# Kernel optimization log

Measured on AMD Instinct MI355X. Metric: run time of the kernel, lower is better.

The kernel has to match this reference:

```python
import jax, jax.numpy as jnp
from jax import lax
import numpy as np

# --- config (torchvision Mask R-CNN RPN / RoIAlign defaults) ---
IMG = 800.0        # image size (square)
STRIDE = 4.0       # FPN level stride -> feature 200x200
K_PRE = 2000       # pre-NMS top-k proposals
K_POST = 512       # post-NMS proposals kept
IOU_THR = 0.7      # RPN NMS IoU threshold
OUT = 7            # RoIAlign output size
SR = 2             # RoIAlign sampling ratio
SCALE = 1.0 / STRIDE
BBOX_XFORM_CLIP = 4.135166556742356  # log(1000/16)


def setup_inputs() -> dict:
    key = jax.random.key(0)
    k1, k2, k3 = jax.random.split(key, 3)
    C, H, W = 256, 200, 200
    feature = jax.random.normal(k1, (C, H, W), jnp.float32)
    # anchor grid: 3 sizes per location, stride 4 (proper geometric anchors)
    sizes = np.array([32.0, 64.0, 128.0], np.float32)
    ys, xs = np.meshgrid(np.arange(H, dtype=np.float32) * STRIDE,
                         np.arange(W, dtype=np.float32) * STRIDE, indexing='ij')
    ctr = np.stack([xs, ys], axis=-1).reshape(-1, 1, 2)            # [HW,1,2] (x,y)
    half = np.stack([sizes / 2, sizes / 2], axis=-1)[None]          # [1,3,2]
    anchors = np.concatenate([ctr - half + 0 * half, ctr + half], axis=-1)
    anchors = np.broadcast_to(np.concatenate([ctr - half, ctr + half], -1),
                              (H * W, 3, 4)).reshape(-1, 4).astype(np.float32)
    N = anchors.shape[0]  # 120000
    objectness = jax.random.normal(k2, (N,), jnp.float32)
    deltas = jax.random.normal(k3, (N, 4), jnp.float32) * 0.1
    return {"feature": feature, "objectness": objectness,
            "deltas": deltas, "anchors": jnp.asarray(anchors)}


def decode_boxes(deltas, anchors):
    w = anchors[:, 2] - anchors[:, 0]
    h = anchors[:, 3] - anchors[:, 1]
    cx = anchors[:, 0] + 0.5 * w
    cy = anchors[:, 1] + 0.5 * h
    dx, dy = deltas[:, 0], deltas[:, 1]
    dw = jnp.minimum(deltas[:, 2], BBOX_XFORM_CLIP)
    dh = jnp.minimum(deltas[:, 3], BBOX_XFORM_CLIP)
    pcx = dx * w + cx
    pcy = dy * h + cy
    pw = jnp.exp(dw) * w
    ph = jnp.exp(dh) * h
    boxes = jnp.stack([pcx - 0.5 * pw, pcy - 0.5 * ph,
                       pcx + 0.5 * pw, pcy + 0.5 * ph], axis=-1)
    return jnp.clip(boxes, 0.0, IMG)


def pairwise_iou(b):  # b: [K,4]
    area = (b[:, 2] - b[:, 0]) * (b[:, 3] - b[:, 1])
    lt = jnp.maximum(b[:, None, :2], b[None, :, :2])
    rb = jnp.minimum(b[:, None, 2:], b[None, :, 2:])
    wh = jnp.maximum(rb - lt, 0.0)
    inter = wh[..., 0] * wh[..., 1]
    return inter / (area[:, None] + area[None, :] - inter + 1e-6)


def nms_suppress(boxes_sorted, iou_thr):
    # boxes sorted by descending score; returns keep mask [K]
    K = boxes_sorted.shape[0]
    iou = pairwise_iou(boxes_sorted)
    js = jnp.arange(K)
    def body(i, supp):
        row = (iou[i] > iou_thr) & (js > i)
        return jnp.where(supp[i], supp, supp | row)
    supp = lax.fori_loop(0, K, body, jnp.zeros((K,), bool))
    return ~supp


def roi_align(feature, boxes):
    # feature: [C,H,W]; boxes: [M,4] in image coords; aligned=False variant
    C, H, W = feature.shape
    P = OUT * SR
    def one(box):
        x1, y1, x2, y2 = box[0] * SCALE, box[1] * SCALE, box[2] * SCALE, box[3] * SCALE
        rw = jnp.maximum(x2 - x1, 1.0)
        rh = jnp.maximum(y2 - y1, 1.0)
        idx = jnp.arange(P, dtype=feature.dtype) + 0.5
        ys = y1 + idx * (rh / P)   # [P]
        xs = x1 + idx * (rw / P)
        yy, xx = jnp.meshgrid(ys, xs, indexing='ij')     # [P,P]
        y = jnp.clip(yy, 0.0, H - 1.0)
        x = jnp.clip(xx, 0.0, W - 1.0)
        y0 = jnp.floor(y).astype(jnp.int32)
        x0 = jnp.floor(x).astype(jnp.int32)
        y1i = jnp.minimum(y0 + 1, H - 1)
        x1i = jnp.minimum(x0 + 1, W - 1)
        ly = y - y0.astype(feature.dtype)
        lx = x - x0.astype(feature.dtype)
        v00 = feature[:, y0, x0]    # [C,P,P]
        v01 = feature[:, y0, x1i]
        v10 = feature[:, y1i, x0]
        v11 = feature[:, y1i, x1i]
        val = (v00 * (1 - ly) * (1 - lx) + v01 * (1 - ly) * lx
               + v10 * ly * (1 - lx) + v11 * ly * lx)  # [C,P,P]
        return val.reshape(C, OUT, SR, OUT, SR).mean(axis=(2, 4))  # [C,7,7]
    return jax.vmap(one)(boxes)


def reference(feature, objectness, deltas, anchors):
    boxes = decode_boxes(deltas, anchors)                    # [N,4]
    scores, idx = lax.top_k(objectness, K_PRE)               # pre-NMS top-k
    cand = boxes[idx]                                        # [K_PRE,4] sorted
    keep = nms_suppress(cand, IOU_THR)                       # [K_PRE] bool
    masked = jnp.where(keep, scores, -jnp.inf)
    _, fidx = lax.top_k(masked, K_POST)                      # post-NMS top-k
    final_boxes = cand[fidx]                                 # [K_POST,4]
    valid = keep[fidx].astype(feature.dtype)                 # [K_POST]
    roi = roi_align(feature, final_boxes)                    # [K_POST,256,7,7]
    return roi * valid[:, None, None, None]
```

## Files before the change

kernel.cpp:

```cpp
#include <hip/hip_runtime.h>
#include <cstdint>
#include <cstddef>

#define N_ANCH   120000
#define K_PRE    2000
#define K_POST   512
#define CAP      4096
#define NWORD    32
#define HBINS    4096
#define IOU_THR  0.7f
#define IMGF     800.0f
#define CLIPV    4.135166556742356f
#define FH       200
#define FW       200
#define FC       256
#define SCALE    0.25f

#define TROWS    96
#define NTILE    21
#define CH       8

#define CG       16
#define TPE      4

typedef unsigned long long u64;
typedef float f2u __attribute__((ext_vector_type(2), aligned(4)));

struct Ws {
    uint32_t T;
    uint32_t cnt;
    int32_t  nk;
    uint32_t pad;
    u64      combo[CAP];
    float4   cand[K_PRE];
    int      rows[K_POST];
    u64      mask[(size_t)K_PRE * NWORD];
};

__device__ inline uint32_t fkey(float f) {
    uint32_t u = __float_as_uint(f);
    return (u & 0x80000000u) ? ~u : (u | 0x80000000u);
}

__global__ __launch_bounds__(1024) void zero_k(Ws* __restrict__ ws) {
    uint32_t* h = (uint32_t*)ws->mask;
    for (int i = threadIdx.x; i < HBINS; i += 1024) h[i] = 0u;
    if (threadIdx.x == 0) { ws->cnt = 0u; ws->nk = 0; ws->T = 0u; }
}

__global__ __launch_bounds__(256) void hist_k(const float* __restrict__ obj,
                                              uint32_t* __restrict__ hist) {
    __shared__ uint32_t h[HBINS];
    for (int i = threadIdx.x; i < HBINS; i += 256) h[i] = 0u;
    __syncthreads();
    const float4* o4 = (const float4*)obj;
    for (int i = blockIdx.x * 256 + threadIdx.x; i < N_ANCH / 4; i += gridDim.x * 256) {
        float4 v = o4[i];
        atomicAdd(&h[fkey(v.x) >> 20], 1u);
        atomicAdd(&h[fkey(v.y) >> 20], 1u);
        atomicAdd(&h[fkey(v.z) >> 20], 1u);
        atomicAdd(&h[fkey(v.w) >> 20], 1u);
    }
    __syncthreads();
    for (int i = threadIdx.x; i < HBINS; i += 256)
        if (h[i]) atomicAdd(&hist[i], h[i]);
}

__global__ __launch_bounds__(256) void gather_k(const float* __restrict__ obj,
                                                const uint32_t* __restrict__ hist,
                                                Ws* __restrict__ ws) {
    __shared__ uint32_t wsum[4];
    __shared__ uint32_t sT;
    const int tid = threadIdx.x;
    const int lane = tid & 63, wave = tid >> 6;
    uint32_t c[16]; uint32_t s = 0;
#pragma unroll
    for (int k = 0; k < 16; ++k) { c[k] = hist[HBINS - 1 - (16 * tid + k)]; s += c[k]; }
    uint32_t incl = s;
    for (int off = 1; off < 64; off <<= 1) {
        uint32_t t = __shfl_up(incl, off);
        if (lane >= off) incl += t;
    }
    if (lane == 63) wsum[wave] = incl;
    __syncthreads();
    uint32_t wpre = 0;
    for (int w2 = 0; w2 < wave; ++w2) wpre += wsum[w2];
    uint32_t before = wpre + incl - s;
#pragma unroll
    for (int k = 0; k < 16; ++k) {
        uint32_t after = before + c[k];
        if (before < K_PRE && after >= K_PRE)
            sT = (uint32_t)(HBINS - 1 - (16 * tid + k)) << 20;
        before = after;
    }
    __syncthreads();
    const uint32_t T = sT;
    int i = blockIdx.x * 256 + tid;
    if (i >= N_ANCH / 4) return;
    float4 v = ((const float4*)obj)[i];
    float vals[4] = {v.x, v.y, v.z, v.w};
#pragma unroll
    for (int k = 0; k < 4; ++k) {
        uint32_t u = fkey(vals[k]);
        if (u >= T) {
            uint32_t pos = atomicAdd(&ws->cnt, 1u);
            if (pos < CAP)
                ws->combo[pos] = ((u64)(~u) << 32) | (uint32_t)(4 * i + k);
        }
    }
}

__global__ __launch_bounds__(256) void rank_decode_k(const float* __restrict__ deltas,
                                                     const float* __restrict__ anchors,
                                                     Ws* __restrict__ ws) {
    __shared__ u64 sc[CAP];
    const int tid = threadIdx.x;
    int M = (int)ws->cnt;
    if (M > CAP) M = CAP;
    const int ebase = blockIdx.x * (256 / TPE);
    if (ebase >= M) return;
    for (int e = tid; e < M; e += 256) sc[e] = ws->combo[e];
    __syncthreads();
    const int gid = ebase + tid / TPE;
    const int sub = tid & (TPE - 1);
    if (gid >= M) return;
    const u64 mine = sc[gid];
    int cnt = 0;
    int j = sub;
    for (; j + 3 * TPE < M; j += 4 * TPE) {
        u64 a = sc[j], b = sc[j + TPE], c = sc[j + 2 * TPE], d = sc[j + 3 * TPE];
        cnt += (int)(a < mine) + (int)(b < mine) + (int)(c < mine) + (int)(d < mine);
    }
    for (; j < M; j += TPE) cnt += (int)(sc[j] < mine);
    cnt += __shfl_xor(cnt, 1);
    cnt += __shfl_xor(cnt, 2);
    if (sub == 0 && cnt < K_PRE) {
        const uint32_t idx = (uint32_t)(mine & 0xFFFFFFFFull);
        float a0 = anchors[idx * 4 + 0], a1 = anchors[idx * 4 + 1];
        float a2 = anchors[idx * 4 + 2], a3 = anchors[idx * 4 + 3];
        float d0 = deltas[idx * 4 + 0],  d1 = deltas[idx * 4 + 1];
        float d2 = fminf(deltas[idx * 4 + 2], CLIPV);
        float d3 = fminf(deltas[idx * 4 + 3], CLIPV);
        float w = a2 - a0, h = a3 - a1;
        float cx = a0 + 0.5f * w, cy = a1 + 0.5f * h;
        float pcx = d0 * w + cx, pcy = d1 * h + cy;
        float pw = expf(d2) * w, ph = expf(d3) * h;
        float x1 = fminf(fmaxf(pcx - 0.5f * pw, 0.0f), IMGF);
        float y1 = fminf(fmaxf(pcy - 0.5f * ph, 0.0f), IMGF);
        float x2 = fminf(fmaxf(pcx + 0.5f * pw, 0.0f), IMGF);
        float y2 = fminf(fmaxf(pcy + 0.5f * ph, 0.0f), IMGF);
        ws->cand[cnt] = make_float4(x1, y1, x2, y2);
    }
}

__global__ __launch_bounds__(256) void nms_mask_k(Ws* __restrict__ ws) {
    const int i = blockIdx.x;
    const int lane = threadIdx.x & 63;
    const int wave = threadIdx.x >> 6;
    const float4 bi = ws->cand[i];
    const float ai = (bi.z - bi.x) * (bi.w - bi.y);
    for (int wd = wave; wd < NWORD; wd += 4) {
        int j = wd * 64 + lane;
        bool bit = false;
        if (j < K_PRE && j > i) {
            float4 bj = ws->cand[j];
            float aj = (bj.z - bj.x) * (bj.w - bj.y);
            float xx1 = fmaxf(bi.x, bj.x);
            float yy1 = fmaxf(bi.y, bj.y);
            float xx2 = fminf(bi.z, bj.z);
            float yy2 = fminf(bi.w, bj.w);
            float ww = fmaxf(xx2 - xx1, 0.0f);
            float hh = fmaxf(yy2 - yy1, 0.0f);
            float inter = ww * hh;
            float iou = inter / (ai + aj - inter + 1e-6f);
            bit = iou > IOU_THR;
        }
        u64 bal = __ballot(bit);
        if (lane == 0) ws->mask[(size_t)i * NWORD + wd] = bal;
    }
}

__global__ __launch_bounds__(512) void nms_scan_k(Ws* __restrict__ ws) {
    __shared__ __align__(16) u64 sbuf[2][TROWS * NWORD];
    __shared__ int s_stop;
    const int tid = threadIdx.x;
    const int lane = tid & 63;
    const int wave = tid >> 6;
    const int lmod = lane & 31;
    const u64* __restrict__ mask = ws->mask;

    {
        const ulonglong2* src = (const ulonglong2*)mask;
        ulonglong2* dst = (ulonglong2*)sbuf[0];
        for (int e = tid; e < TROWS * NWORD / 2; e += 512) dst[e] = src[e];
    }
    if (tid == 0) s_stop = 0;
    __syncthreads();

    u64 supp = 0ull;
    int kcnt = 0;
    int decided = 0;
    for (int t = 0; t < NTILE; ++t) {
        const int base = t * TROWS;
        const int nb = min(TROWS, K_PRE - base);
        if (wave == 0) {
            const u64* sm = sbuf[t & 1];
            u64 A[CH], B[CH];
#pragma unroll
            for (int b = 0; b < CH; ++b) A[b] = sm[b * NWORD + lmod];
            for (int s = 0; s < nb; s += 2 * CH) {
                const bool hasB = (s + CH) < nb;
                if (hasB) {
#pragma unroll
                    for (int b = 0; b < CH; ++b) B[b] = sm[(s + CH + b) * NWORD + lmod];
                }
                {
                    const int w = (base + s) >> 6;
                    const int bofs = (base + s) & 63;
                    u64 keptw = 0ull;
                    if (lane == w) {
                        u64 cur = supp;
#pragma unroll
                        for (int b = 0; b < CH; ++b) {
                            u64 bit = (cur >> (bofs + b)) & 1ull;
                            u64 sel = bit - 1ull;
                            cur |= A[b] & sel;
                            keptw |= sel & (1ull << b);
                        }
                        supp = cur;
                    }
                    u64 kb = __shfl(keptw, w);
                    kcnt += __popcll(kb);
#pragma unroll
                    for (int b = 0; b < CH; ++b) {
                        u64 sel = 0ull - ((kb >> b) & 1ull);
                        supp |= A[b] & sel;
                    }
                }
                if (hasB) {
                    if (s + 2 * CH < nb) {
#pragma unroll
                        for (int b = 0; b < CH; ++b)
                            A[b] = sm[(s + 2 * CH + b) * NWORD + lmod];
                    }
                    const int w = (base + s + CH) >> 6;
                    const int bofs = (base + s + CH) & 63;
                    u64 keptw = 0ull;
                    if (lane == w) {
                        u64 cur = supp;
#pragma unroll
                        for (int b = 0; b < CH; ++b) {
                            u64 bit = (cur >> (bofs + b)) & 1ull;
                            u64 sel = bit - 1ull;
                            cur |= B[b] & sel;
                            keptw |= sel & (1ull << b);
                        }
                        supp = cur;
                    }
                    u64 kb = __shfl(keptw, w);
                    kcnt += __popcll(kb);
#pragma unroll
                    for (int b = 0; b < CH; ++b) {
                        u64 sel = 0ull - ((kb >> b) & 1ull);
                        supp |= B[b] & sel;
                    }
                }
            }
            decided = base + nb;
            if (lane == 0 && kcnt >= K_POST) s_stop = 1;
        } else if (t + 1 < NTILE) {
            const int nbase = (t + 1) * TROWS;
            const int npairs = (min(TROWS, K_PRE - nbase) * NWORD) / 2;
            const ulonglong2* src = (const ulonglong2*)(mask + (size_t)nbase * NWORD);
            ulonglong2* dst = (ulonglong2*)sbuf[(t + 1) & 1];
            for (int e = tid - 64; e < npairs; e += 448) dst[e] = src[e];
        }
        __syncthreads();
        if (s_stop) break;
    }

    if (wave == 0) {
        u64 valid;
        if (lane < NWORD - 1)       valid = ~0ull;
        else if (lane == NWORD - 1) valid = (1ull << (K_PRE - (NWORD - 1) * 64)) - 1ull;
        else                        valid = 0ull;
        const int dw = decided - lane * 64;
        const u64 dmask = (dw <= 0) ? 0ull : ((dw >= 64) ? ~0ull : ((1ull << dw) - 1ull));
        u64 keepw = (~supp) & valid & dmask;
        int cnt = __popcll(keepw);
        int incl = cnt;
        for (int off = 1; off < 64; off <<= 1) {
            int t = __shfl_up(incl, off);
            if (lane >= off) incl += t;
        }
        int pos = incl - cnt;
        u64 kw = keepw;
        while (kw) {
            int b = __ffsll((unsigned long long)kw) - 1;
            kw &= kw - 1ull;
            if (pos < K_POST) ws->rows[pos] = lane * 64 + b;
            ++pos;
        }
        int total = __shfl(incl, 63);
        if (lane == 0) ws->nk = total;
        int start = total < K_POST ? total : K_POST;
        for (int r = start + lane; r < K_POST; r += 64) ws->rows[r] = -1;
    }
}

__global__ __launch_bounds__(256) void roi_k(const float* __restrict__ feat,
                                             const Ws* __restrict__ ws,
                                             float* __restrict__ out) {
    const int b = blockIdx.x;
    const int xcd = b & 7;
    const int s = b >> 3;
    const int r = s & (K_POST - 1);
    const int cg = xcd + 8 * (s >> 9);
    const int cbase = cg * CG;
    float* oblk = out + (size_t)r * (FC * 49) + (size_t)cbase * 49;
    const int row = ws->rows[r];
    const int tid = threadIdx.x;

    if (row < 0) {
        for (int e = tid; e < CG * 49; e += 256) oblk[e] = 0.0f;
        return;
    }
    if (tid >= 245) return;

    const int p = tid % 49;
    const int cslot = tid / 49;
    const int oy = p / 7, ox = p % 7;

    const float4 bx = ws->cand[row];
    const float x1 = bx.x * SCALE, y1 = bx.y * SCALE;
    const float x2 = bx.z * SCALE, y2 = bx.w * SCALE;
    const float rw = fmaxf(x2 - x1, 1.0f);
    const float rh = fmaxf(y2 - y1, 1.0f);
    const float stepx = rw / 14.0f;
    const float stepy = rh / 14.0f;

    int    off0[4], off1[4];
    float4 w4[4];
#pragma unroll
    for (int sub = 0; sub < 4; ++sub) {
        const int sy = sub >> 1, sx = sub & 1;
        float yy = y1 + ((float)(2 * oy + sy) + 0.5f) * stepy;
        float y = fminf(fmaxf(yy, 0.0f), (float)(FH - 1));
        float fy0 = floorf(y);
        int iy0 = (int)fy0;
        int iy1 = min(iy0 + 1, FH - 1);
        float ly = y - fy0;
        float xx = x1 + ((float)(2 * ox + sx) + 0.5f) * stepx;
        float x = fminf(fmaxf(xx, 0.0f), (float)(FW - 1));
        float fx0 = floorf(x);
        int ix0 = (int)fx0;
        float lx = x - fx0;
        float wxl, wxr; int base;
        if (ix0 >= FW - 1) { base = FW - 2; wxl = 0.0f; wxr = 1.0f; }
        else               { base = ix0;    wxl = 1.0f - lx; wxr = lx; }
        float wy0 = 1.0f - ly, wy1 = ly;
        off0[sub] = iy0 * FW + base;
        off1[sub] = iy1 * FW + base;
        w4[sub] = make_float4(wy0 * wxl * 0.25f, wy0 * wxr * 0.25f,
                              wy1 * wxl * 0.25f, wy1 * wxr * 0.25f);
    }

    const float* fb = feat + (size_t)cbase * (FH * FW);
    const float* f0 = fb + (size_t)cslot * (FH * FW);
    const float* f1 = fb + (size_t)(cslot + 5) * (FH * FW);
    const float* f2 = fb + (size_t)(cslot + 10) * (FH * FW);
    f2u r0[8], r1[8], r2[8], r3[8];
#pragma unroll
    for (int sub = 0; sub < 4; ++sub) {
        r0[2 * sub]     = *(const f2u*)(f0 + off0[sub]);
        r0[2 * sub + 1] = *(const f2u*)(f0 + off1[sub]);
    }
#pragma unroll
    for (int sub = 0; sub < 4; ++sub) {
        r1[2 * sub]     = *(const f2u*)(f1 + off0[sub]);
        r1[2 * sub + 1] = *(const f2u*)(f1 + off1[sub]);
    }
#pragma unroll
    for (int sub = 0; sub < 4; ++sub) {
        r2[2 * sub]     = *(const f2u*)(f2 + off0[sub]);
        r2[2 * sub + 1] = *(const f2u*)(f2 + off1[sub]);
    }
    const bool has4 = (cslot == 0);
    if (has4) {
        const float* f3 = fb + (size_t)15 * (FH * FW);
#pragma unroll
        for (int sub = 0; sub < 4; ++sub) {
            r3[2 * sub]     = *(const f2u*)(f3 + off0[sub]);
            r3[2 * sub + 1] = *(const f2u*)(f3 + off1[sub]);
        }
    }

    float a0 = 0.0f, a1 = 0.0f, a2 = 0.0f;
#pragma unroll
    for (int sub = 0; sub < 4; ++sub) {
        a0 += w4[sub].x * r0[2 * sub].x + w4[sub].y * r0[2 * sub].y
            + w4[sub].z * r0[2 * sub + 1].x + w4[sub].w * r0[2 * sub + 1].y;
    }
#pragma unroll
    for (int sub = 0; sub < 4; ++sub) {
        a1 += w4[sub].x * r1[2 * sub].x + w4[sub].y * r1[2 * sub].y
            + w4[sub].z * r1[2 * sub + 1].x + w4[sub].w * r1[2 * sub + 1].y;
    }
#pragma unroll
    for (int sub = 0; sub < 4; ++sub) {
        a2 += w4[sub].x * r2[2 * sub].x + w4[sub].y * r2[2 * sub].y
            + w4[sub].z * r2[2 * sub + 1].x + w4[sub].w * r2[2 * sub + 1].y;
    }
    oblk[cslot * 49 + p] = a0;
    oblk[(cslot + 5) * 49 + p] = a1;
    oblk[(cslot + 10) * 49 + p] = a2;

    if (has4) {
        float a3 = 0.0f;
#pragma unroll
        for (int sub = 0; sub < 4; ++sub) {
            a3 += w4[sub].x * r3[2 * sub].x + w4[sub].y * r3[2 * sub].y
                + w4[sub].z * r3[2 * sub + 1].x + w4[sub].w * r3[2 * sub + 1].y;
        }
        oblk[15 * 49 + p] = a3;
    }
}

extern "C" void kernel_launch(void* const* d_in, const int* in_sizes, int n_in,
                              void* d_out, int out_size, void* d_ws, size_t ws_size,
                              hipStream_t stream) {
    const float* feature    = (const float*)d_in[0];
    const float* objectness = (const float*)d_in[1];
    const float* deltas     = (const float*)d_in[2];
    const float* anchors    = (const float*)d_in[3];
    Ws* ws = (Ws*)d_ws;
    uint32_t* hist = (uint32_t*)ws->mask;
    float* out = (float*)d_out;

    hipLaunchKernelGGL(zero_k, dim3(1), dim3(1024), 0, stream, ws);
    hipLaunchKernelGGL(hist_k, dim3(256), dim3(256), 0, stream, objectness, hist);
    hipLaunchKernelGGL(gather_k, dim3((N_ANCH / 4 + 255) / 256), dim3(256), 0, stream,
                       objectness, hist, ws);
    hipLaunchKernelGGL(rank_decode_k, dim3(CAP / (256 / TPE)), dim3(256), 0, stream,
                       deltas, anchors, ws);
    hipLaunchKernelGGL(nms_mask_k, dim3(K_PRE), dim3(256), 0, stream, ws);
    hipLaunchKernelGGL(nms_scan_k, dim3(1), dim3(512), 0, stream, ws);
    hipLaunchKernelGGL(roi_k, dim3(16 * K_POST), dim3(256), 0, stream, feature, ws, out);
}
```

Measured before the change: 195.2 us.

## Fuse selection stages into one grid-synced kernel and merge mask with scan

Replaces the zero, histogram, gather and rank/decode kernels with a single 128-block kernel that uses global atomic-counter barriers between phases. The NMS mask and scan kernels are merged using a last-block-done pattern, where the final finishing block runs the sequential scan. This removes several kernel launches and the gaps between them. In exchange it relies on all 128 blocks being co-resident for the spin barriers, adds a memset, and reuses ws->T as the completion counter.

```diff
diff --git a/kernel.cpp b/kernel.cpp
--- a/kernel.cpp
+++ b/kernel.cpp
@@ -22,6 +22,7 @@
 
 #define CG       16
 #define TPE      4
+#define SEL_NB   128
 
 typedef unsigned long long u64;
 typedef float f2u __attribute__((ext_vector_type(2), aligned(4)));
@@ -42,153 +43,191 @@
     return (u & 0x80000000u) ? ~u : (u | 0x80000000u);
 }
 
-__global__ __launch_bounds__(1024) void zero_k(Ws* __restrict__ ws) {
-    uint32_t* h = (uint32_t*)ws->mask;
-    for (int i = threadIdx.x; i < HBINS; i += 1024) h[i] = 0u;
-    if (threadIdx.x == 0) { ws->cnt = 0u; ws->nk = 0; ws->T = 0u; }
-}
-
-__global__ __launch_bounds__(256) void hist_k(const float* __restrict__ obj,
-                                              uint32_t* __restrict__ hist) {
-    __shared__ uint32_t h[HBINS];
-    for (int i = threadIdx.x; i < HBINS; i += 256) h[i] = 0u;
-    __syncthreads();
-    const float4* o4 = (const float4*)obj;
-    for (int i = blockIdx.x * 256 + threadIdx.x; i < N_ANCH / 4; i += gridDim.x * 256) {
-        float4 v = o4[i];
-        atomicAdd(&h[fkey(v.x) >> 20], 1u);
-        atomicAdd(&h[fkey(v.y) >> 20], 1u);
-        atomicAdd(&h[fkey(v.z) >> 20], 1u);
-        atomicAdd(&h[fkey(v.w) >> 20], 1u);
-    }
-    __syncthreads();
-    for (int i = threadIdx.x; i < HBINS; i += 256)
-        if (h[i]) atomicAdd(&hist[i], h[i]);
-}
-
-__global__ __launch_bounds__(256) void gather_k(const float* __restrict__ obj,
-                                                const uint32_t* __restrict__ hist,
-                                                Ws* __restrict__ ws) {
-    __shared__ uint32_t wsum[4];
-    __shared__ uint32_t sT;
-    const int tid = threadIdx.x;
-    const int lane = tid & 63, wave = tid >> 6;
-    uint32_t c[16]; uint32_t s = 0;
-#pragma unroll
-    for (int k = 0; k < 16; ++k) { c[k] = hist[HBINS - 1 - (16 * tid + k)]; s += c[k]; }
-    uint32_t incl = s;
-    for (int off = 1; off < 64; off <<= 1) {
-        uint32_t t = __shfl_up(incl, off);
-        if (lane >= off) incl += t;
-    }
-    if (lane == 63) wsum[wave] = incl;
-    __syncthreads();
-    uint32_t wpre = 0;
-    for (int w2 = 0; w2 < wave; ++w2) wpre += wsum[w2];
-    uint32_t before = wpre + incl - s;
-#pragma unroll
-    for (int k = 0; k < 16; ++k) {
-        uint32_t after = before + c[k];
-        if (before < K_PRE && after >= K_PRE)
-            sT = (uint32_t)(HBINS - 1 - (16 * tid + k)) << 20;
-        before = after;
-    }
-    __syncthreads();
-    const uint32_t T = sT;
-    int i = blockIdx.x * 256 + tid;
-    if (i >= N_ANCH / 4) return;
-    float4 v = ((const float4*)obj)[i];
-    float vals[4] = {v.x, v.y, v.z, v.w};
-#pragma unroll
-    for (int k = 0; k < 4; ++k) {
-        uint32_t u = fkey(vals[k]);
-        if (u >= T) {
-            uint32_t pos = atomicAdd(&ws->cnt, 1u);
-            if (pos < CAP)
-                ws->combo[pos] = ((u64)(~u) << 32) | (uint32_t)(4 * i + k);
-        }
-    }
-}
-
-__global__ __launch_bounds__(256) void rank_decode_k(const float* __restrict__ deltas,
-                                                     const float* __restrict__ anchors,
-                                                     Ws* __restrict__ ws) {
-    __shared__ u64 sc[CAP];
-    const int tid = threadIdx.x;
-    int M = (int)ws->cnt;
-    if (M > CAP) M = CAP;
-    const int ebase = blockIdx.x * (256 / TPE);
-    if (ebase >= M) return;
-    for (int e = tid; e < M; e += 256) sc[e] = ws->combo[e];
-    __syncthreads();
-    const int gid = ebase + tid / TPE;
-    const int sub = tid & (TPE - 1);
-    if (gid >= M) return;
-    const u64 mine = sc[gid];
-    int cnt = 0;
-    int j = sub;
-    for (; j + 3 * TPE < M; j += 4 * TPE) {
-        u64 a = sc[j], b = sc[j + TPE], c = sc[j + 2 * TPE], d = sc[j + 3 * TPE];
-        cnt += (int)(a < mine) + (int)(b < mine) + (int)(c < mine) + (int)(d < mine);
-    }
-    for (; j < M; j += TPE) cnt += (int)(sc[j] < mine);
-    cnt += __shfl_xor(cnt, 1);
-    cnt += __shfl_xor(cnt, 2);
-    if (sub == 0 && cnt < K_PRE) {
-        const uint32_t idx = (uint32_t)(mine & 0xFFFFFFFFull);
-        float a0 = anchors[idx * 4 + 0], a1 = anchors[idx * 4 + 1];
-        float a2 = anchors[idx * 4 + 2], a3 = anchors[idx * 4 + 3];
-        float d0 = deltas[idx * 4 + 0],  d1 = deltas[idx * 4 + 1];
-        float d2 = fminf(deltas[idx * 4 + 2], CLIPV);
-        float d3 = fminf(deltas[idx * 4 + 3], CLIPV);
-        float w = a2 - a0, h = a3 - a1;
-        float cx = a0 + 0.5f * w, cy = a1 + 0.5f * h;
-        float pcx = d0 * w + cx, pcy = d1 * h + cy;
-        float pw = expf(d2) * w, ph = expf(d3) * h;
-        float x1 = fminf(fmaxf(pcx - 0.5f * pw, 0.0f), IMGF);
-        float y1 = fminf(fmaxf(pcy - 0.5f * ph, 0.0f), IMGF);
-        float x2 = fminf(fmaxf(pcx + 0.5f * pw, 0.0f), IMGF);
-        float y2 = fminf(fmaxf(pcy + 0.5f * ph, 0.0f), IMGF);
-        ws->cand[cnt] = make_float4(x1, y1, x2, y2);
-    }
-}
-
-__global__ __launch_bounds__(256) void nms_mask_k(Ws* __restrict__ ws) {
-    const int i = blockIdx.x;
-    const int lane = threadIdx.x & 63;
-    const int wave = threadIdx.x >> 6;
-    const float4 bi = ws->cand[i];
-    const float ai = (bi.z - bi.x) * (bi.w - bi.y);
-    for (int wd = wave; wd < NWORD; wd += 4) {
-        int j = wd * 64 + lane;
-        bool bit = false;
-        if (j < K_PRE && j > i) {
-            float4 bj = ws->cand[j];
-            float aj = (bj.z - bj.x) * (bj.w - bj.y);
-            float xx1 = fmaxf(bi.x, bj.x);
-            float yy1 = fmaxf(bi.y, bj.y);
-            float xx2 = fminf(bi.z, bj.z);
-            float yy2 = fminf(bi.w, bj.w);
-            float ww = fmaxf(xx2 - xx1, 0.0f);
-            float hh = fmaxf(yy2 - yy1, 0.0f);
-            float inter = ww * hh;
-            float iou = inter / (ai + aj - inter + 1e-6f);
-            bit = iou > IOU_THR;
-        }
-        u64 bal = __ballot(bit);
-        if (lane == 0) ws->mask[(size_t)i * NWORD + wd] = bal;
-    }
-}
-
-__global__ __launch_bounds__(512) void nms_scan_k(Ws* __restrict__ ws) {
+__device__ inline void dbar(uint32_t* ctr, uint32_t nb) {
+    __syncthreads();
+    if (threadIdx.x == 0) {
+        __threadfence();
+        atomicAdd(ctr, 1u);
+        while (__hip_atomic_load(ctr, __ATOMIC_RELAXED, __HIP_MEMORY_SCOPE_AGENT) < nb)
+            __builtin_amdgcn_s_sleep(2);
+        __threadfence();
+    }
+    __syncthreads();
+}
+
+union __align__(16) SelSmem {
+    uint32_t hist[HBINS];
+    struct { uint32_t wsum[4]; uint32_t sT; } res;
+    u64 sc[CAP];
+};
+
+__global__ __launch_bounds__(256) void sel_k(const float* __restrict__ obj,
+                                             const float* __restrict__ deltas,
+                                             const float* __restrict__ anchors,
+                                             Ws* __restrict__ ws) {
+    __shared__ SelSmem sm;
+    const int tid  = threadIdx.x;
+    const int bid  = blockIdx.x;
+    const int lane = tid & 63;
+    const int wave = tid >> 6;
+    uint32_t* hist = (uint32_t*)ws->mask;
+    uint32_t* bctr = hist + HBINS;
+
+    if (tid < HBINS / SEL_NB) hist[bid * (HBINS / SEL_NB) + tid] = 0u;
+    if (bid == 0 && tid == 0) { ws->cnt = 0u; ws->T = 0u; }
+
+    for (int i = tid; i < HBINS; i += 256) sm.hist[i] = 0u;
+    __syncthreads();
+    {
+        const float4* o4 = (const float4*)obj;
+        const int i = bid * 256 + tid;
+        if (i < N_ANCH / 4) {
+            float4 v = o4[i];
+            atomicAdd(&sm.hist[fkey(v.x) >> 20], 1u);
+            atomicAdd(&sm.hist[fkey(v.y) >> 20], 1u);
+            atomicAdd(&sm.hist[fkey(v.z) >> 20], 1u);
+            atomicAdd(&sm.hist[fkey(v.w) >> 20], 1u);
+        }
+    }
+    __syncthreads();
+
+    dbar(&bctr[0], SEL_NB);
+
+    for (int i = tid; i < HBINS; i += 256)
+        if (sm.hist[i]) atomicAdd(&hist[i], sm.hist[i]);
+
+    dbar(&bctr[1], SEL_NB);
+
+    {
+        uint32_t c[16]; uint32_t s = 0;
+#pragma unroll
+        for (int k = 0; k < 16; ++k) { c[k] = hist[HBINS - 1 - (16 * tid + k)]; s += c[k]; }
+        uint32_t incl = s;
+        for (int off = 1; off < 64; off <<= 1) {
+            uint32_t t = __shfl_up(incl, off);
+            if (lane >= off) incl += t;
+        }
+        __syncthreads();
+        if (lane == 63) sm.res.wsum[wave] = incl;
+        __syncthreads();
+        uint32_t wpre = 0;
+        for (int w2 = 0; w2 < wave; ++w2) wpre += sm.res.wsum[w2];
+        uint32_t before = wpre + incl - s;
+#pragma unroll
+        for (int k = 0; k < 16; ++k) {
+            uint32_t after = before + c[k];
+            if (before < K_PRE && after >= K_PRE)
+                sm.res.sT = (uint32_t)(HBINS - 1 - (16 * tid + k)) << 20;
+            before = after;
+        }
+        __syncthreads();
+        const uint32_t T = sm.res.sT;
+        const int i = bid * 256 + tid;
+        if (i < N_ANCH / 4) {
+            float4 v = ((const float4*)obj)[i];
+            float vals[4] = {v.x, v.y, v.z, v.w};
+#pragma unroll
+            for (int k = 0; k < 4; ++k) {
+                uint32_t u = fkey(vals[k]);
+                if (u >= T) {
+                    uint32_t pos = atomicAdd(&ws->cnt, 1u);
+                    if (pos < CAP)
+                        ws->combo[pos] = ((u64)(~u) << 32) | (uint32_t)(4 * i + k);
+                }
+            }
+        }
+    }
+
+    dbar(&bctr[2], SEL_NB);
+
+    {
+        int M = (int)ws->cnt;
+        if (M > CAP) M = CAP;
+        const int ebase = bid * (256 / TPE);
+        if (ebase >= M) return;
+        __syncthreads();
+        for (int e = tid; e < M; e += 256) sm.sc[e] = ws->combo[e];
+        __syncthreads();
+        const int gid = ebase + tid / TPE;
+        const int sub = tid & (TPE - 1);
+        if (gid >= M) return;
+        const u64 mine = sm.sc[gid];
+        int cnt = 0;
+        int j = sub;
+        for (; j + 3 * TPE < M; j += 4 * TPE) {
+            u64 a = sm.sc[j], b = sm.sc[j + TPE];
+            u64 c2 = sm.sc[j + 2 * TPE], d = sm.sc[j + 3 * TPE];
+            cnt += (int)(a < mine) + (int)(b < mine) + (int)(c2 < mine) + (int)(d < mine);
+        }
+        for (; j < M; j += TPE) cnt += (int)(sm.sc[j] < mine);
+        cnt += __shfl_xor(cnt, 1);
+        cnt += __shfl_xor(cnt, 2);
+        if (sub == 0 && cnt < K_PRE) {
+            const uint32_t idx = (uint32_t)(mine & 0xFFFFFFFFull);
+            float a0 = anchors[idx * 4 + 0], a1 = anchors[idx * 4 + 1];
+            float a2 = anchors[idx * 4 + 2], a3 = anchors[idx * 4 + 3];
+            float d0 = deltas[idx * 4 + 0],  d1 = deltas[idx * 4 + 1];
+            float d2 = fminf(deltas[idx * 4 + 2], CLIPV);
+            float d3 = fminf(deltas[idx * 4 + 3], CLIPV);
+            float w = a2 - a0, h = a3 - a1;
+            float cx = a0 + 0.5f * w, cy = a1 + 0.5f * h;
+            float pcx = d0 * w + cx, pcy = d1 * h + cy;
+            float pw = expf(d2) * w, ph = expf(d3) * h;
+            float x1 = fminf(fmaxf(pcx - 0.5f * pw, 0.0f), IMGF);
+            float y1 = fminf(fmaxf(pcy - 0.5f * ph, 0.0f), IMGF);
+            float x2 = fminf(fmaxf(pcx + 0.5f * pw, 0.0f), IMGF);
+            float y2 = fminf(fmaxf(pcy + 0.5f * ph, 0.0f), IMGF);
+            ws->cand[cnt] = make_float4(x1, y1, x2, y2);
+        }
+    }
+}
+
+__global__ __launch_bounds__(512) void mask_scan_k(Ws* __restrict__ ws) {
     __shared__ __align__(16) u64 sbuf[2][TROWS * NWORD];
     __shared__ int s_stop;
+    __shared__ int s_last;
     const int tid = threadIdx.x;
     const int lane = tid & 63;
     const int wave = tid >> 6;
+
+    {
+        const int i = blockIdx.x;
+        const float4 bi = ws->cand[i];
+        const float ai = (bi.z - bi.x) * (bi.w - bi.y);
+        for (int wd = wave; wd < NWORD; wd += 8) {
+            int j = wd * 64 + lane;
+            bool bit = false;
+            if (j < K_PRE && j > i) {
+                float4 bj = ws->cand[j];
+                float aj = (bj.z - bj.x) * (bj.w - bj.y);
+                float xx1 = fmaxf(bi.x, bj.x);
+                float yy1 = fmaxf(bi.y, bj.y);
+                float xx2 = fminf(bi.z, bj.z);
+                float yy2 = fminf(bi.w, bj.w);
+                float ww = fmaxf(xx2 - xx1, 0.0f);
+                float hh = fmaxf(yy2 - yy1, 0.0f);
+                float inter = ww * hh;
+                float iou = inter / (ai + aj - inter + 1e-6f);
+                bit = iou > IOU_THR;
+            }
+            u64 bal = __ballot(bit);
+            if (lane == 0) ws->mask[(size_t)i * NWORD + wd] = bal;
+        }
+    }
+
+    __syncthreads();
+    if (tid == 0) {
+        __threadfence();
+        uint32_t old = atomicAdd(&ws->T, 1u);
+        s_last = (old == K_PRE - 1) ? 1 : 0;
+    }
+    __syncthreads();
+    if (!s_last) return;
+    if (tid == 0) __threadfence();
+    __syncthreads();
+
     const int lmod = lane & 31;
     const u64* __restrict__ mask = ws->mask;
-
     {
         const ulonglong2* src = (const ulonglong2*)mask;
         ulonglong2* dst = (ulonglong2*)sbuf[0];
@@ -434,16 +473,12 @@
     const float* deltas     = (const float*)d_in[2];
     const float* anchors    = (const float*)d_in[3];
     Ws* ws = (Ws*)d_ws;
-    uint32_t* hist = (uint32_t*)ws->mask;
     float* out = (float*)d_out;
 
-    hipLaunchKernelGGL(zero_k, dim3(1), dim3(1024), 0, stream, ws);
-    hipLaunchKernelGGL(hist_k, dim3(256), dim3(256), 0, stream, objectness, hist);
-    hipLaunchKernelGGL(gather_k, dim3((N_ANCH / 4 + 255) / 256), dim3(256), 0, stream,
-                       objectness, hist, ws);
-    hipLaunchKernelGGL(rank_decode_k, dim3(CAP / (256 / TPE)), dim3(256), 0, stream,
-                       deltas, anchors, ws);
-    hipLaunchKernelGGL(nms_mask_k, dim3(K_PRE), dim3(256), 0, stream, ws);
-    hipLaunchKernelGGL(nms_scan_k, dim3(1), dim3(512), 0, stream, ws);
+    hipMemsetAsync((char*)d_ws + offsetof(Ws, mask) + (size_t)HBINS * 4, 0, 12, stream);
+
+    hipLaunchKernelGGL(sel_k, dim3(SEL_NB), dim3(256), 0, stream,
+                       objectness, deltas, anchors, ws);
+    hipLaunchKernelGGL(mask_scan_k, dim3(K_PRE), dim3(512), 0, stream, ws);
     hipLaunchKernelGGL(roi_k, dim3(16 * K_POST), dim3(256), 0, stream, feature, ws, out);
 }
```

Result: slower. 252.1 us (+29.2%).

## Fuse NMS scan with RoIAlign via progressive row publishing and spin-wait

Applied to the files above, without the earlier changes.

Merges the serial NMS scan kernel and the RoIAlign kernel into one launch. Block 0 runs the scan and, after each tile, publishes the kept rows found so far together with an atomic release counter. The remaining blocks spin on that counter until their row is ready, then run RoIAlign, so feature gathering overlaps the scan. RoI blocks now cover two channel groups with 512 threads each. This relies on block 0 being scheduled, or on enough other blocks finishing, to avoid deadlock, and the spinning blocks occupy compute units while they wait.

```diff
diff --git a/kernel.cpp b/kernel.cpp
--- a/kernel.cpp
+++ b/kernel.cpp
@@ -180,155 +180,182 @@
     }
 }
 
-__global__ __launch_bounds__(512) void nms_scan_k(Ws* __restrict__ ws) {
+__global__ __launch_bounds__(512) void scan_roi_k(const float* __restrict__ feat,
+                                                  Ws* __restrict__ ws,
+                                                  float* __restrict__ out) {
     __shared__ __align__(16) u64 sbuf[2][TROWS * NWORD];
     __shared__ int s_stop;
+    __shared__ int sRow;
     const int tid = threadIdx.x;
     const int lane = tid & 63;
     const int wave = tid >> 6;
-    const int lmod = lane & 31;
-    const u64* __restrict__ mask = ws->mask;
-
-    {
-        const ulonglong2* src = (const ulonglong2*)mask;
-        ulonglong2* dst = (ulonglong2*)sbuf[0];
-        for (int e = tid; e < TROWS * NWORD / 2; e += 512) dst[e] = src[e];
-    }
-    if (tid == 0) s_stop = 0;
-    __syncthreads();
-
-    u64 supp = 0ull;
-    int kcnt = 0;
-    int decided = 0;
-    for (int t = 0; t < NTILE; ++t) {
-        const int base = t * TROWS;
-        const int nb = min(TROWS, K_PRE - base);
-        if (wave == 0) {
-            const u64* sm = sbuf[t & 1];
-            u64 A[CH], B[CH];
-#pragma unroll
-            for (int b = 0; b < CH; ++b) A[b] = sm[b * NWORD + lmod];
-            for (int s = 0; s < nb; s += 2 * CH) {
-                const bool hasB = (s + CH) < nb;
-                if (hasB) {
-#pragma unroll
-                    for (int b = 0; b < CH; ++b) B[b] = sm[(s + CH + b) * NWORD + lmod];
+
+    if (blockIdx.x == 0) {
+        const int lmod = lane & 31;
+        const u64* __restrict__ mask = ws->mask;
+        {
+            const ulonglong2* src = (const ulonglong2*)mask;
+            ulonglong2* dst = (ulonglong2*)sbuf[0];
+            for (int e = tid; e < TROWS * NWORD / 2; e += 512) dst[e] = src[e];
+        }
+        if (tid == 0) s_stop = 0;
+        __syncthreads();
+
+        u64 supp = 0ull;
+        int pubtot = 0;
+        const u64 valid = (lane < NWORD - 1) ? ~0ull
+                        : (lane == NWORD - 1 ? ((1ull << (K_PRE - (NWORD - 1) * 64)) - 1ull)
+                                             : 0ull);
+        for (int t = 0; t < NTILE; ++t) {
+            const int base = t * TROWS;
+            const int nb = min(TROWS, K_PRE - base);
+            if (wave == 0) {
+                const u64* sm = sbuf[t & 1];
+                u64 A[CH], B[CH];
+#pragma unroll
+                for (int b = 0; b < CH; ++b) A[b] = sm[b * NWORD + lmod];
+                for (int s = 0; s < nb; s += 2 * CH) {
+                    const bool hasB = (s + CH) < nb;
+                    if (hasB) {
+#pragma unroll
+                        for (int b = 0; b < CH; ++b) B[b] = sm[(s + CH + b) * NWORD + lmod];
+                    }
+                    {
+                        const int w = (base + s) >> 6;
+                        const int bofs = (base + s) & 63;
+                        u64 keptw = 0ull;
+                        if (lane == w) {
+                            u64 cur = supp;
+#pragma unroll
+                            for (int b = 0; b < CH; ++b) {
+                                u64 bit = (cur >> (bofs + b)) & 1ull;
+                                u64 sel = bit - 1ull;
+                                cur |= A[b] & sel;
+                                keptw |= sel & (1ull << b);
+                            }
+                            supp = cur;
+                        }
+                        u64 kb = __shfl(keptw, w);
+#pragma unroll
+                        for (int b = 0; b < CH; ++b) {
+                            u64 sel = 0ull - ((kb >> b) & 1ull);
+                            supp |= A[b] & sel;
+                        }
+                    }
+                    if (hasB) {
+                        if (s + 2 * CH < nb) {
+#pragma unroll
+                            for (int b = 0; b < CH; ++b)
+                                A[b] = sm[(s + 2 * CH + b) * NWORD + lmod];
+                        }
+                        const int w = (base + s + CH) >> 6;
+                        const int bofs = (base + s + CH) & 63;
+                        u64 keptw = 0ull;
+                        if (lane == w) {
+                            u64 cur = supp;
+#pragma unroll
+                            for (int b = 0; b < CH; ++b) {
+                                u64 bit = (cur >> (bofs + b)) & 1ull;
+                                u64 sel = bit - 1ull;
+                                cur |= B[b] & sel;
+                                keptw |= sel & (1ull << b);
+                            }
+                            supp = cur;
+                        }
+                        u64 kb = __shfl(keptw, w);
+#pragma unroll
+                        for (int b = 0; b < CH; ++b) {
+                            u64 sel = 0ull - ((kb >> b) & 1ull);
+                            supp |= B[b] & sel;
+                        }
+                    }
                 }
                 {
-                    const int w = (base + s) >> 6;
-                    const int bofs = (base + s) & 63;
-                    u64 keptw = 0ull;
-                    if (lane == w) {
-                        u64 cur = supp;
-#pragma unroll
-                        for (int b = 0; b < CH; ++b) {
-                            u64 bit = (cur >> (bofs + b)) & 1ull;
-                            u64 sel = bit - 1ull;
-                            cur |= A[b] & sel;
-                            keptw |= sel & (1ull << b);
-                        }
-                        supp = cur;
-                    }
-                    u64 kb = __shfl(keptw, w);
-                    kcnt += __popcll(kb);
-#pragma unroll
-                    for (int b = 0; b < CH; ++b) {
-                        u64 sel = 0ull - ((kb >> b) & 1ull);
-                        supp |= A[b] & sel;
+                    const int w0 = lane << 6;
+                    int lo = base - w0;      if (lo < 0)  lo = 0;
+                    int hi = base + nb - w0; if (hi > 64) hi = 64;
+                    u64 rmask = 0ull;
+                    if (hi > lo) {
+                        u64 mh = (hi >= 64) ? ~0ull : ((1ull << hi) - 1ull);
+                        u64 ml = (lo <= 0) ? 0ull : ((1ull << lo) - 1ull);
+                        rmask = mh & ~ml;
+                    }
+                    u64 keepn = (~supp) & valid & rmask;
+                    int c = __popcll(keepn);
+                    int incl = c;
+                    for (int off = 1; off < 64; off <<= 1) {
+                        int tt = __shfl_up(incl, off);
+                        if (lane >= off) incl += tt;
+                    }
+                    int pos = pubtot + incl - c;
+                    u64 kw = keepn;
+                    while (kw) {
+                        int b = __ffsll((unsigned long long)kw) - 1;
+                        kw &= kw - 1ull;
+                        if (pos < K_POST)
+                            __hip_atomic_store(&ws->rows[pos], w0 + b,
+                                               __ATOMIC_RELAXED, __HIP_MEMORY_SCOPE_AGENT);
+                        ++pos;
+                    }
+                    pubtot += __shfl(incl, 63);
+                    int pr = pubtot < K_POST ? pubtot : K_POST;
+                    if (lane == 0) {
+                        __hip_atomic_store(&ws->T, (uint32_t)pr,
+                                           __ATOMIC_RELEASE, __HIP_MEMORY_SCOPE_AGENT);
+                        if (pubtot >= K_POST) s_stop = 1;
                     }
                 }
-                if (hasB) {
-                    if (s + 2 * CH < nb) {
-#pragma unroll
-                        for (int b = 0; b < CH; ++b)
-                            A[b] = sm[(s + 2 * CH + b) * NWORD + lmod];
-                    }
-                    const int w = (base + s + CH) >> 6;
-                    const int bofs = (base + s + CH) & 63;
-                    u64 keptw = 0ull;
-                    if (lane == w) {
-                        u64 cur = supp;
-#pragma unroll
-                        for (int b = 0; b < CH; ++b) {
-                            u64 bit = (cur >> (bofs + b)) & 1ull;
-                            u64 sel = bit - 1ull;
-                            cur |= B[b] & sel;
-                            keptw |= sel & (1ull << b);
-                        }
-                        supp = cur;
-                    }
-                    u64 kb = __shfl(keptw, w);
-                    kcnt += __popcll(kb);
-#pragma unroll
-                    for (int b = 0; b < CH; ++b) {
-                        u64 sel = 0ull - ((kb >> b) & 1ull);
-                        supp |= B[b] & sel;
-                    }
-                }
+            } else if (t + 1 < NTILE) {
+                const int nbase = (t + 1) * TROWS;
+                const int npairs = (min(TROWS, K_PRE - nbase) * NWORD) / 2;
+                const ulonglong2* src = (const ulonglong2*)(mask + (size_t)nbase * NWORD);
+                ulonglong2* dst = (ulonglong2*)sbuf[(t + 1) & 1];
+                for (int e = tid - 64; e < npairs; e += 448) dst[e] = src[e];
             }
-            decided = base + nb;
-            if (lane == 0 && kcnt >= K_POST) s_stop = 1;
-        } else if (t + 1 < NTILE) {
-            const int nbase = (t + 1) * TROWS;
-            const int npairs = (min(TROWS, K_PRE - nbase) * NWORD) / 2;
-            const ulonglong2* src = (const ulonglong2*)(mask + (size_t)nbase * NWORD);
-            ulonglong2* dst = (ulonglong2*)sbuf[(t + 1) & 1];
-            for (int e = tid - 64; e < npairs; e += 448) dst[e] = src[e];
-        }
-        __syncthreads();
-        if (s_stop) break;
-    }
-
-    if (wave == 0) {
-        u64 valid;
-        if (lane < NWORD - 1)       valid = ~0ull;
-        else if (lane == NWORD - 1) valid = (1ull << (K_PRE - (NWORD - 1) * 64)) - 1ull;
-        else                        valid = 0ull;
-        const int dw = decided - lane * 64;
-        const u64 dmask = (dw <= 0) ? 0ull : ((dw >= 64) ? ~0ull : ((1ull << dw) - 1ull));
-        u64 keepw = (~supp) & valid & dmask;
-        int cnt = __popcll(keepw);
-        int incl = cnt;
-        for (int off = 1; off < 64; off <<= 1) {
-            int t = __shfl_up(incl, off);
-            if (lane >= off) incl += t;
-        }
-        int pos = incl - cnt;
-        u64 kw = keepw;
-        while (kw) {
-            int b = __ffsll((unsigned long long)kw) - 1;
-            kw &= kw - 1ull;
-            if (pos < K_POST) ws->rows[pos] = lane * 64 + b;
-            ++pos;
-        }
-        int total = __shfl(incl, 63);
-        if (lane == 0) ws->nk = total;
-        int start = total < K_POST ? total : K_POST;
-        for (int r = start + lane; r < K_POST; r += 64) ws->rows[r] = -1;
-    }
-}
-
-__global__ __launch_bounds__(256) void roi_k(const float* __restrict__ feat,
-                                             const Ws* __restrict__ ws,
-                                             float* __restrict__ out) {
-    const int b = blockIdx.x;
-    const int xcd = b & 7;
-    const int s = b >> 3;
-    const int r = s & (K_POST - 1);
-    const int cg = xcd + 8 * (s >> 9);
+            __syncthreads();
+            if (s_stop) break;
+        }
+
+        if (wave == 0) {
+            for (int rr = pubtot + lane; rr < K_POST; rr += 64)
+                __hip_atomic_store(&ws->rows[rr], -1,
+                                   __ATOMIC_RELAXED, __HIP_MEMORY_SCOPE_AGENT);
+            if (lane == 0) {
+                ws->nk = pubtot;
+                __hip_atomic_store(&ws->T, (uint32_t)K_POST,
+                                   __ATOMIC_RELEASE, __HIP_MEMORY_SCOPE_AGENT);
+            }
+        }
+        return;
+    }
+
+    const int u = (int)blockIdx.x - 1;
+    const int r = u >> 3;
+    const int xcd = u & 7;
+    const int h = tid >> 8;
+    const int tid2 = tid & 255;
+    const int cg = xcd + 8 * h;
     const int cbase = cg * CG;
+
+    if (tid == 0) {
+        while (__hip_atomic_load(&ws->T, __ATOMIC_RELAXED, __HIP_MEMORY_SCOPE_AGENT)
+               <= (uint32_t)r)
+            __builtin_amdgcn_s_sleep(16);
+        (void)__hip_atomic_load(&ws->T, __ATOMIC_ACQUIRE, __HIP_MEMORY_SCOPE_AGENT);
+        sRow = __hip_atomic_load(&ws->rows[r], __ATOMIC_RELAXED, __HIP_MEMORY_SCOPE_AGENT);
+    }
+    __syncthreads();
+    const int row = sRow;
     float* oblk = out + (size_t)r * (FC * 49) + (size_t)cbase * 49;
-    const int row = ws->rows[r];
-    const int tid = threadIdx.x;
 
     if (row < 0) {
-        for (int e = tid; e < CG * 49; e += 256) oblk[e] = 0.0f;
+        for (int e = tid2; e < CG * 49; e += 256) oblk[e] = 0.0f;
         return;
     }
-    if (tid >= 245) return;
-
-    const int p = tid % 49;
-    const int cslot = tid / 49;
+    if (tid2 >= 245) return;
+
+    const int p = tid2 % 49;
+    const int cslot = tid2 / 49;
     const int oy = p / 7, ox = p % 7;
 
     const float4 bx = ws->cand[row];
@@ -444,6 +471,6 @@
     hipLaunchKernelGGL(rank_decode_k, dim3(CAP / (256 / TPE)), dim3(256), 0, stream,
                        deltas, anchors, ws);
     hipLaunchKernelGGL(nms_mask_k, dim3(K_PRE), dim3(256), 0, stream, ws);
-    hipLaunchKernelGGL(nms_scan_k, dim3(1), dim3(512), 0, stream, ws);
-    hipLaunchKernelGGL(roi_k, dim3(16 * K_POST), dim3(256), 0, stream, feature, ws, out);
-}
+    hipLaunchKernelGGL(scan_roi_k, dim3(1 + 8 * K_POST), dim3(512), 0, stream,
+                       feature, ws, out);
+}
```

New measurement: 200.8 us. 2.8% more time.

## Transpose feature map to HWC fused with histogram, use channel-vectorized RoIAlign

Applied to the files above, without the earlier changes.

Adds a kernel that transposes the CHW feature map into an HWC copy in workspace and also does the objectness histogram in the same launch. A new RoIAlign kernel reads float4 channel groups from the HWC layout for each bilinear corner, then stages the results in shared memory so the output writes are coalesced. The goal is to replace scattered per-channel gathers with contiguous vector loads. The cost is an extra full feature-map read and write (about 41 MB) on every call, and the path only runs when the workspace is large enough.

```diff
diff --git a/kernel.cpp b/kernel.cpp
--- a/kernel.cpp
+++ b/kernel.cpp
@@ -23,6 +23,7 @@
 #define CG       16
 #define TPE      4
 
+
 typedef unsigned long long u64;
 typedef float f2u __attribute__((ext_vector_type(2), aligned(4)));
 
@@ -46,6 +47,41 @@
     uint32_t* h = (uint32_t*)ws->mask;
     for (int i = threadIdx.x; i < HBINS; i += 1024) h[i] = 0u;
     if (threadIdx.x == 0) { ws->cnt = 0u; ws->nk = 0; ws->T = 0u; }
+}
+
+__global__ __launch_bounds__(256) void th_k(const float* __restrict__ feat,
+                                            const float* __restrict__ obj,
+                                            float* __restrict__ featT,
+                                            uint32_t* __restrict__ hist) {
+    __shared__ float tile[32][257];
+    __shared__ uint32_t h[HBINS];
+    const int tid = threadIdx.x, bid = blockIdx.x;
+
+    if (bid < 118) {
+        for (int i = tid; i < HBINS; i += 256) h[i] = 0u;
+        __syncthreads();
+        const int i = bid * 256 + tid;
+        if (i < N_ANCH / 4) {
+            float4 v = ((const float4*)obj)[i];
+            atomicAdd(&h[fkey(v.x) >> 20], 1u);
+            atomicAdd(&h[fkey(v.y) >> 20], 1u);
+            atomicAdd(&h[fkey(v.z) >> 20], 1u);
+            atomicAdd(&h[fkey(v.w) >> 20], 1u);
+        }
+        __syncthreads();
+        for (int i2 = tid; i2 < HBINS; i2 += 256)
+            if (h[i2]) atomicAdd(&hist[i2], h[i2]);
+    }
+
+    const int P0 = bid * 32;
+    const int pl = tid & 31, c0 = tid >> 5;
+#pragma unroll
+    for (int k = 0; k < 32; ++k)
+        tile[pl][k * 8 + c0] = feat[(size_t)(k * 8 + c0) * (FH * FW) + P0 + pl];
+    __syncthreads();
+#pragma unroll
+    for (int m = 0; m < 32; ++m)
+        featT[(size_t)(P0 + m) * FC + tid] = tile[m][tid];
 }
 
 __global__ __launch_bounds__(256) void hist_k(const float* __restrict__ obj,
@@ -308,6 +344,92 @@
     }
 }
 
+__global__ __launch_bounds__(256) void roi2_k(const float* __restrict__ featT,
+                                              const Ws* __restrict__ ws,
+                                              float* __restrict__ out) {
+    __shared__ float sout[CG * 49];
+    const int b = blockIdx.x;
+    const int xcd = b & 7;
+    const int s = b >> 3;
+    const int r = s & (K_POST - 1);
+    const int cg = xcd + 8 * (s >> 9);
+    const int cbase = cg * CG;
+    float* oblk = out + (size_t)r * (FC * 49) + (size_t)cbase * 49;
+    const int row = ws->rows[r];
+    const int tid = threadIdx.x;
+
+    if (row < 0) {
+        for (int e = tid; e < CG * 49; e += 256) oblk[e] = 0.0f;
+        return;
+    }
+
+    if (tid < 196) {
+        const int p = tid >> 2;
+        const int cq = tid & 3;
+        const int oy = p / 7, ox = p % 7;
+
+        const float4 bx = ws->cand[row];
+        const float x1 = bx.x * SCALE, y1 = bx.y * SCALE;
+        const float x2 = bx.z * SCALE, y2 = bx.w * SCALE;
+        const float rw = fmaxf(x2 - x1, 1.0f);
+        const float rh = fmaxf(y2 - y1, 1.0f);
+        const float stepx = rw / 14.0f;
+        const float stepy = rh / 14.0f;
+
+        int    o0[4], o1[4];
+        float4 w4[4];
+#pragma unroll
+        for (int sub = 0; sub < 4; ++sub) {
+            const int sy = sub >> 1, sx = sub & 1;
+            float yy = y1 + ((float)(2 * oy + sy) + 0.5f) * stepy;
+            float y = fminf(fmaxf(yy, 0.0f), (float)(FH - 1));
+            float fy0 = floorf(y);
+            int iy0 = (int)fy0;
+            int iy1 = min(iy0 + 1, FH - 1);
+            float ly = y - fy0;
+            float xx = x1 + ((float)(2 * ox + sx) + 0.5f) * stepx;
+            float x = fminf(fmaxf(xx, 0.0f), (float)(FW - 1));
+            float fx0 = floorf(x);
+            int ix0 = (int)fx0;
+            float lx = x - fx0;
+            float wxl, wxr; int basex;
+            if (ix0 >= FW - 1) { basex = FW - 2; wxl = 0.0f; wxr = 1.0f; }
+            else               { basex = ix0;    wxl = 1.0f - lx; wxr = lx; }
+            float wy0 = 1.0f - ly, wy1 = ly;
+            o0[sub] = (iy0 * FW + basex) * FC;
+            o1[sub] = (iy1 * FW + basex) * FC;
+            w4[sub] = make_float4(wy0 * wxl * 0.25f, wy0 * wxr * 0.25f,
+                                  wy1 * wxl * 0.25f, wy1 * wxr * 0.25f);
+        }
+
+        const int cofs = cbase + cq * 4;
+        float4 v[16];
+#pragma unroll
+        for (int sub = 0; sub < 4; ++sub) {
+            v[4 * sub + 0] = *(const float4*)(featT + (size_t)o0[sub] + cofs);
+            v[4 * sub + 1] = *(const float4*)(featT + (size_t)o0[sub] + FC + cofs);
+            v[4 * sub + 2] = *(const float4*)(featT + (size_t)o1[sub] + cofs);
+            v[4 * sub + 3] = *(const float4*)(featT + (size_t)o1[sub] + FC + cofs);
+        }
+
+        float ax = 0.0f, ay = 0.0f, az = 0.0f, aw = 0.0f;
+#pragma unroll
+        for (int sub = 0; sub < 4; ++sub) {
+            const float4 w = w4[sub];
+            ax += w.x * v[4*sub].x + w.y * v[4*sub+1].x + w.z * v[4*sub+2].x + w.w * v[4*sub+3].x;
+            ay += w.x * v[4*sub].y + w.y * v[4*sub+1].y + w.z * v[4*sub+2].y + w.w * v[4*sub+3].y;
+            az += w.x * v[4*sub].z + w.y * v[4*sub+1].z + w.z * v[4*sub+2].z + w.w * v[4*sub+3].z;
+            aw += w.x * v[4*sub].w + w.y * v[4*sub+1].w + w.z * v[4*sub+2].w + w.w * v[4*sub+3].w;
+        }
+        sout[(cq * 4 + 0) * 49 + p] = ax;
+        sout[(cq * 4 + 1) * 49 + p] = ay;
+        sout[(cq * 4 + 2) * 49 + p] = az;
+        sout[(cq * 4 + 3) * 49 + p] = aw;
+    }
+    __syncthreads();
+    for (int e = tid; e < CG * 49; e += 256) oblk[e] = sout[e];
+}
+
 __global__ __launch_bounds__(256) void roi_k(const float* __restrict__ feat,
                                              const Ws* __restrict__ ws,
                                              float* __restrict__ out) {
@@ -437,13 +559,29 @@
     uint32_t* hist = (uint32_t*)ws->mask;
     float* out = (float*)d_out;
 
+    const size_t ftOff = (sizeof(Ws) + 255) & ~(size_t)255;
+    const size_t need  = ftOff + (size_t)(FH * FW) * FC * sizeof(float);
+    const bool hwc = (ws_size >= need);
+    float* featT = (float*)((char*)d_ws + ftOff);
+
     hipLaunchKernelGGL(zero_k, dim3(1), dim3(1024), 0, stream, ws);
-    hipLaunchKernelGGL(hist_k, dim3(256), dim3(256), 0, stream, objectness, hist);
+    if (hwc) {
+        hipLaunchKernelGGL(th_k, dim3(FH * FW / 32), dim3(256), 0, stream,
+                           feature, objectness, featT, hist);
+    } else {
+        hipLaunchKernelGGL(hist_k, dim3(256), dim3(256), 0, stream, objectness, hist);
+    }
     hipLaunchKernelGGL(gather_k, dim3((N_ANCH / 4 + 255) / 256), dim3(256), 0, stream,
                        objectness, hist, ws);
     hipLaunchKernelGGL(rank_decode_k, dim3(CAP / (256 / TPE)), dim3(256), 0, stream,
                        deltas, anchors, ws);
     hipLaunchKernelGGL(nms_mask_k, dim3(K_PRE), dim3(256), 0, stream, ws);
     hipLaunchKernelGGL(nms_scan_k, dim3(1), dim3(512), 0, stream, ws);
-    hipLaunchKernelGGL(roi_k, dim3(16 * K_POST), dim3(256), 0, stream, feature, ws, out);
-}
+    if (hwc) {
+        hipLaunchKernelGGL(roi2_k, dim3(16 * K_POST), dim3(256), 0, stream,
+                           featT, ws, out);
+    } else {
+        hipLaunchKernelGGL(roi_k, dim3(16 * K_POST), dim3(256), 0, stream,
+                           feature, ws, out);
+    }
+}
```

New measurement: 208.0 us. 6.5% more time.
